# Optimization experiments

Measured on AMD Instinct MI355X. Metric: run time of the kernel, lower is better.

## Reference

```python
import jax, jax.numpy as jnp
import numpy as np

D_MODEL, D_STATE, EXPAND = 768, 16, 2
D_INNER = D_MODEL * EXPAND
B, L = 2, 2048


def setup_inputs() -> dict:
    key = jax.random.key(0)
    ks = jax.random.split(key, 10)
    s = 0.02  # init scale for projection weights
    return {
        "x": jax.random.normal(ks[0], (B, L, D_MODEL), jnp.float32),
        "in_w": jax.random.normal(ks[1], (D_MODEL, 2 * D_INNER), jnp.float32) * s,
        "conv_w": jax.random.normal(ks[2], (D_INNER, 1, 3), jnp.float32) * 0.1,
        "conv_b": jnp.zeros((D_INNER,), jnp.float32),
        "xproj_w": jax.random.normal(ks[3], (D_INNER, 2 * D_STATE), jnp.float32) * s,
        "dt_w": jax.random.normal(ks[4], (D_INNER, D_INNER), jnp.float32) * s,
        "dt_b": jnp.zeros((D_INNER,), jnp.float32),
        "A_log": jax.random.normal(ks[5], (D_INNER, D_STATE), jnp.float32) * 0.01,
        "D": jnp.ones((D_INNER,), jnp.float32),
        "out_w": jax.random.normal(ks[6], (D_INNER, D_MODEL), jnp.float32) * s,
    }


def reference(x, in_w, conv_w, conv_b, xproj_w, dt_w, dt_b, A_log, D, out_w):
    d_inner = conv_w.shape[0]
    d_state = A_log.shape[1]

    xz = x @ in_w                                   # [B,L,2*d_inner]
    x_c, z = jnp.split(xz, 2, axis=-1)

    # depthwise conv1d, kernel 3, padding 1
    xc = jnp.transpose(x_c, (0, 2, 1))              # [B,d_inner,L]
    xc = jax.lax.conv_general_dilated(
        xc, conv_w, window_strides=(1,), padding=[(1, 1)],
        feature_group_count=d_inner,
        dimension_numbers=("NCH", "OIH", "NCH"))
    xc = xc + conv_b[None, :, None]
    xc = jax.nn.silu(jnp.transpose(xc, (0, 2, 1)))  # [B,L,d_inner]

    Bs, Cs = jnp.split(xc @ xproj_w, 2, axis=-1)    # each [B,L,d_state]
    delta = jax.nn.softplus(xc @ dt_w + dt_b)       # [B,L,d_inner]
    A = -jnp.exp(A_log.astype(jnp.float32))         # [d_inner,d_state]

    deltaA = jnp.exp(jnp.einsum("bld,dn->bldn", delta, A))      # [B,L,d_inner,d_state]
    deltaBx = jnp.einsum("bld,bln->bldn", delta * xc, Bs)        # [B,L,d_inner,d_state]

    def step(h, inp):
        dA_t, dBx_t, c_t = inp                      # [B,d,n],[B,d,n],[B,n]
        h = dA_t * h + dBx_t
        y_t = jnp.einsum("bdn,bn->bd", h, c_t)
        return h, y_t

    h0 = jnp.zeros((x.shape[0], d_inner, d_state), xc.dtype)
    xs = (jnp.moveaxis(deltaA, 1, 0), jnp.moveaxis(deltaBx, 1, 0), jnp.moveaxis(Cs, 1, 0))
    _, ys = jax.lax.scan(step, h0, xs)              # ys: [L,B,d_inner]
    y = jnp.moveaxis(ys, 0, 1) + D * xc             # skip connection

    y = y * jax.nn.silu(z)
    return y @ out_w                                # [B,L,d_model]
```

## Files before the change

### kernel.cpp

```cpp
#include <hip/hip_runtime.h>
#include <cmath>

#define DMODEL 768
#define DINNER 1536
#define NSTATE 16
#define SEQL   2048
#define NCHUNK 32
#define CHLEN  64

#define DT_F32  0
#define DT_BF16 1
#define DT_ZERO 2

typedef __bf16 bf16x8 __attribute__((ext_vector_type(8)));
typedef float  f32x4  __attribute__((ext_vector_type(4)));

typedef __attribute__((address_space(3))) unsigned short lds_us;
typedef const __attribute__((address_space(1))) unsigned short glob_us;

__device__ __forceinline__ void async_cp16(glob_us* g, lds_us* l) {
    __builtin_amdgcn_global_load_lds((const __attribute__((address_space(1))) void*)g,
                                     (__attribute__((address_space(3))) void*)l, 16, 0, 0);
}

__device__ __forceinline__ float bf2f(unsigned short h) {
    union { unsigned u; float f; } v; v.u = ((unsigned)h) << 16; return v.f;
}
__device__ __forceinline__ unsigned short f2bf(float f) {
    union { float f; unsigned u; } v; v.f = f;
    unsigned r = (v.u + 0x7FFFu + ((v.u >> 16) & 1u)) >> 16;
    return (unsigned short)r;
}
__device__ int detect_dtype(const void* p) {
    const unsigned* u = (const unsigned*)p;
    int nzlo = 0, band = 0, anynz = 0;
    for (int i = 0; i < 64; ++i) {
        unsigned w = u[i];
        anynz |= (w != 0);
        unsigned lo = w & 0xFFFFu;
        if (lo) {
            ++nzlo;
            unsigned e8 = (lo >> 7) & 0xFF;
            if (e8 >= 0x60 && e8 <= 0x8E) ++band;
        }
    }
    if (nzlo >= 8) return (band * 2 > nzlo) ? DT_BF16 : DT_F32;
    return anynz ? DT_F32 : DT_ZERO;
}
__device__ __forceinline__ float LD(const void* p, size_t i, int dt) {
    if (dt == DT_BF16) return bf2f(((const unsigned short*)p)[i]);
    if (dt == DT_F32)  return ((const float*)p)[i];
    return 0.f;
}

__global__ __launch_bounds__(256) void prep_kernel(
    const void* __restrict__ x, const void* __restrict__ in_w,
    const void* __restrict__ cw, const void* __restrict__ cb,
    const void* __restrict__ xp, const void* __restrict__ dt_w,
    const void* __restrict__ db, const void* __restrict__ Al,
    const void* __restrict__ Dv, const void* __restrict__ out_w,
    unsigned short* __restrict__ xb, unsigned short* __restrict__ inT,
    unsigned short* __restrict__ dtT, unsigned short* __restrict__ outT,
    float* __restrict__ pf)
{
    __shared__ unsigned short tile[64][68];
    __shared__ int dts[6];
    const int blk = blockIdx.x;
    const int t   = threadIdx.x;

    if (blk < 324) {
        if (t == 0) {
            dts[0] = detect_dtype(cw); dts[1] = detect_dtype(cb);
            dts[2] = detect_dtype(db); dts[3] = detect_dtype(Al);
            dts[4] = detect_dtype(Dv); dts[5] = detect_dtype(xp);
        }
        __syncthreads();
        int g = blk * 256 + t;
        if (g >= 82944) return;
        const void* src; int local; int which;
        if      (g <  4608) { src = cw; local = g;         which = 0; }
        else if (g <  6144) { src = cb; local = g - 4608;  which = 1; }
        else if (g <  7680) { src = db; local = g - 6144;  which = 2; }
        else if (g < 32256) { src = Al; local = g - 7680;  which = 3; }
        else if (g < 33792) { src = Dv; local = g - 32256; which = 4; }
        else                { src = xp; local = g - 33792; which = 5; }
        float v = LD(src, local, dts[which]);
        if (which == 3) v = -__expf(v) * 1.44269504f;
        pf[g] = v;
    } else if (blk < 1860) {
        if (t == 0) dts[0] = detect_dtype(x);
        __syncthreads();
        const int dt = dts[0];
        size_t i = ((size_t)(blk - 324) * 256 + t) * 8;
        ushort4 o0, o1;
        if (dt == DT_F32) {
            float4 a = *(const float4*)((const float*)x + i);
            float4 b = *(const float4*)((const float*)x + i + 4);
            o0.x = f2bf(a.x); o0.y = f2bf(a.y); o0.z = f2bf(a.z); o0.w = f2bf(a.w);
            o1.x = f2bf(b.x); o1.y = f2bf(b.y); o1.z = f2bf(b.z); o1.w = f2bf(b.w);
        } else if (dt == DT_BF16) {
            o0 = *(const ushort4*)((const unsigned short*)x + i);
            o1 = *(const ushort4*)((const unsigned short*)x + i + 4);
        } else {
            o0 = (ushort4){0,0,0,0}; o1 = (ushort4){0,0,0,0};
        }
        *(ushort4*)&xb[i] = o0;
        *(ushort4*)&xb[i + 4] = o1;
    } else {
        const void* src; unsigned short* dst; int R, C, tx_n, idx;
        if (blk < 2436)      { src = in_w;  dst = inT;  R = 768;  C = 3072; tx_n = 48; idx = blk - 1860; }
        else if (blk < 3012) { src = dt_w;  dst = dtT;  R = 1536; C = 1536; tx_n = 24; idx = blk - 2436; }
        else                 { src = out_w; dst = outT; R = 1536; C = 768;  tx_n = 12; idx = blk - 3012; }
        if (t == 0) dts[0] = detect_dtype(src);
        __syncthreads();
        const int dt = dts[0];
        const int tx = t & 15, ty = t >> 4;
        const int bx = (idx % tx_n) * 64, by = (idx / tx_n) * 64;
        #pragma unroll
        for (int i = 0; i < 4; ++i) {
            int rl = ty + i * 16;
            size_t soff = (size_t)(by + rl) * C + bx + tx * 4;
            ushort4 hv;
            if (dt == DT_F32) {
                float4 v = *(const float4*)((const float*)src + soff);
                hv.x = f2bf(v.x); hv.y = f2bf(v.y); hv.z = f2bf(v.z); hv.w = f2bf(v.w);
            } else if (dt == DT_BF16) {
                hv = *(const ushort4*)((const unsigned short*)src + soff);
            } else {
                hv = (ushort4){0,0,0,0};
            }
            *(ushort4*)&tile[rl][tx * 4] = hv;
        }
        __syncthreads();
        #pragma unroll
        for (int i = 0; i < 4; ++i) {
            int cl = ty + i * 16;
            int m0 = tx * 4;
            ushort4 o;
            o.x = tile[m0 + 0][cl]; o.y = tile[m0 + 1][cl];
            o.z = tile[m0 + 2][cl]; o.w = tile[m0 + 3][cl];
            *(ushort4*)&dst[(size_t)(bx + cl) * R + by + m0] = o;
        }
    }
}

template<int EPI>
__global__ __launch_bounds__(256) void gemm_kernel(
    const unsigned short* __restrict__ A, const unsigned short* __restrict__ Bt,
    void* __restrict__ C0, void* __restrict__ C1, const float* __restrict__ biasf,
    int M, int N, int K)
{
    __shared__ __align__(16) unsigned short As[2][2][128 * 32];
    __shared__ __align__(16) unsigned short Bs[2][2][64 * 32];
    const int t    = threadIdx.x;
    const int m0   = blockIdx.x * 128;
    const int n0   = blockIdx.y * 64;
    const int w    = t >> 6;
    const int lane = t & 63;
    const int wm   = (w >> 1) * 64, wn = (w & 1) * 32;
    const int lm   = lane & 15, quad = lane >> 4;
    const int srow = lane >> 2;
    const int sg   = lane & 3;

    f32x4 acc[4][2] = {};

    auto stage = [&](int k0, int q) {
        #pragma unroll
        for (int ph = 0; ph < 2; ++ph) {
            #pragma unroll
            for (int h = 0; h < 2; ++h) {
                int row = w * 32 + h * 16 + srow;
                int kg  = (sg - (row >> 1)) & 3;
                async_cp16((glob_us*)&A[(size_t)(m0 + row) * K + k0 + ph * 32 + kg * 8],
                           (lds_us*)&As[q][ph][(w * 32 + h * 16) * 32]);
            }
            int brow = w * 16 + srow;
            int bkg  = (sg - (brow >> 1)) & 3;
            async_cp16((glob_us*)&Bt[(size_t)(n0 + brow) * K + k0 + ph * 32 + bkg * 8],
                       (lds_us*)&Bs[q][ph][(w * 16) * 32]);
        }
    };

    stage(0, 0);

    int p = 0;
    for (int k0 = 0; k0 < K; k0 += 64) {
        __syncthreads();
        if (k0 + 64 < K) stage(k0 + 64, p ^ 1);
        #pragma unroll
        for (int ph = 0; ph < 2; ++ph) {
            bf16x8 af[4], bfr[2];
            #pragma unroll
            for (int i = 0; i < 4; ++i) {
                int row = wm + i * 16 + lm;
                int g   = (quad + (row >> 1)) & 3;
                af[i] = *(const bf16x8*)&As[p][ph][row * 32 + g * 8];
            }
            #pragma unroll
            for (int j = 0; j < 2; ++j) {
                int row = wn + j * 16 + lm;
                int g   = (quad + (row >> 1)) & 3;
                bfr[j] = *(const bf16x8*)&Bs[p][ph][row * 32 + g * 8];
            }
            #pragma unroll
            for (int i = 0; i < 4; ++i)
                #pragma unroll
                for (int j = 0; j < 2; ++j)
                    acc[i][j] = __builtin_amdgcn_mfma_f32_16x16x32_bf16(af[i], bfr[j], acc[i][j], 0, 0, 0);
        }
        p ^= 1;
    }

    const int half = N >> 1;
    #pragma unroll
    for (int i = 0; i < 4; ++i) {
        #pragma unroll
        for (int j = 0; j < 2; ++j) {
            int col = n0 + wn + j * 16 + lm;
            #pragma unroll
            for (int r = 0; r < 4; ++r) {
                int row = m0 + wm + i * 16 + quad * 4 + r;
                float v = acc[i][j][r];
                if (EPI == 1) {
                    v += biasf[col];
                    float sp = (v > 20.f) ? v : log1pf(__expf(v));
                    ((unsigned short*)C0)[(size_t)row * N + col] = f2bf(sp);
                } else if (EPI == 2) {
                    ((float*)C0)[(size_t)row * N + col] = v;
                } else {
                    if (col < half) {
                        ((unsigned short*)C0)[(size_t)row * half + col] = f2bf(v);
                    } else {
                        float s = v / (1.f + __expf(-v));
                        ((unsigned short*)C1)[(size_t)row * half + col - half] = f2bf(s);
                    }
                }
            }
        }
    }
}

__global__ __launch_bounds__(256) void conv_silu_kernel(
    const unsigned short* __restrict__ xcpre, const float* __restrict__ cwf,
    const float* __restrict__ cbf, unsigned short* __restrict__ xcb)
{
    int idx = blockIdx.x * 256 + threadIdx.x;
    int d   = idx % DINNER;
    int row = idx / DINNER;
    int l   = row % SEQL;
    size_t base = (size_t)row * DINNER + d;
    float acc = cbf[d];
    if (l > 0)        acc += bf2f(xcpre[base - DINNER]) * cwf[d * 3 + 0];
    acc += bf2f(xcpre[base]) * cwf[d * 3 + 1];
    if (l < SEQL - 1) acc += bf2f(xcpre[base + DINNER]) * cwf[d * 3 + 2];
    float s = acc / (1.f + __expf(-acc));
    xcb[base] = f2bf(s);
}

__global__ __launch_bounds__(128) void xproj_kernel(
    const unsigned short* __restrict__ xcb, const float* __restrict__ wf,
    float* __restrict__ BC)
{
    __shared__ float red[4][32][4];
    const int t = threadIdx.x;
    const int s = t & 31, part = t >> 5;
    const int row0 = blockIdx.x * 4;
    float acc[4] = {0.f, 0.f, 0.f, 0.f};
    for (int k = part * 384; k < (part + 1) * 384; ++k) {
        float wv = wf[k * 32 + s];
        #pragma unroll
        for (int r = 0; r < 4; ++r)
            acc[r] += bf2f(xcb[(size_t)(row0 + r) * DINNER + k]) * wv;
    }
    #pragma unroll
    for (int r = 0; r < 4; ++r) red[part][s][r] = acc[r];
    __syncthreads();
    if (t < 32) {
        #pragma unroll
        for (int r = 0; r < 4; ++r)
            BC[(size_t)(row0 + r) * 32 + t] =
                red[0][t][r] + red[1][t][r] + red[2][t][r] + red[3][t][r];
    }
}

struct GrpA { unsigned short dv[4], xv[4]; f32x4 Bv[4]; };
struct GrpC { unsigned short dv[4], xv[4], zq; f32x4 Bv[4], Cv[4]; };

__device__ __forceinline__ void ldA(GrpA& gp, const unsigned short* pd,
    const unsigned short* px, const float* pbc, int l) {
    #pragma unroll
    for (int j = 0; j < 4; ++j) {
        size_t o = (size_t)(l + j) * DINNER;
        gp.dv[j] = pd[o];
        gp.xv[j] = px[o];
        gp.Bv[j] = *(const f32x4*)&pbc[(size_t)(l + j) * 32];
    }
}
__device__ __forceinline__ void ldC(GrpC& gp, const unsigned short* pd,
    const unsigned short* px, const unsigned short* pz, const float* pbc,
    int l, int q) {
    #pragma unroll
    for (int j = 0; j < 4; ++j) {
        size_t o = (size_t)(l + j) * DINNER;
        gp.dv[j] = pd[o];
        gp.xv[j] = px[o];
        gp.Bv[j] = *(const f32x4*)&pbc[(size_t)(l + j) * 32];
        gp.Cv[j] = *(const f32x4*)&pbc[(size_t)(l + j) * 32 + 16];
    }
    gp.zq = pz[(size_t)(l + q) * DINNER];
}
__device__ __forceinline__ void stepA(const GrpA& gp, const f32x4 A2,
    f32x4& h, float& sdv) {
    #pragma unroll
    for (int j = 0; j < 4; ++j) {
        float dv = bf2f(gp.dv[j]);
        float xv = bf2f(gp.xv[j]);
        float dx = dv * xv;
        sdv += dv;
        f32x4 e;
        e[0] = __builtin_amdgcn_exp2f(dv * A2[0]);
        e[1] = __builtin_amdgcn_exp2f(dv * A2[1]);
        e[2] = __builtin_amdgcn_exp2f(dv * A2[2]);
        e[3] = __builtin_amdgcn_exp2f(dv * A2[3]);
        h = e * h + dx * gp.Bv[j];
    }
}
__device__ __forceinline__ void stepC(const GrpC& gp, const f32x4 A2,
    f32x4& h, float Dd, int q, unsigned short* py, int l) {
    float yq = 0.f, xq = 0.f;
    #pragma unroll
    for (int j = 0; j < 4; ++j) {
        float dv = bf2f(gp.dv[j]);
        float xv = bf2f(gp.xv[j]);
        float dx = dv * xv;
        f32x4 e;
        e[0] = __builtin_amdgcn_exp2f(dv * A2[0]);
        e[1] = __builtin_amdgcn_exp2f(dv * A2[1]);
        e[2] = __builtin_amdgcn_exp2f(dv * A2[2]);
        e[3] = __builtin_amdgcn_exp2f(dv * A2[3]);
        h = e * h + dx * gp.Bv[j];
        f32x4 yv = h * gp.Cv[j];
        float y = yv[0] + yv[1] + yv[2] + yv[3];
        y += __shfl_xor(y, 1);
        y += __shfl_xor(y, 2);
        if (j == q) { yq = y; xq = xv; }
    }
    float zv = bf2f(gp.zq);
    py[(size_t)(l + q) * DINNER] = f2bf((yq + Dd * xq) * zv);
}

__global__ __launch_bounds__(256) void scan_phase_a(
    const unsigned short* __restrict__ dlt, const unsigned short* __restrict__ xcb,
    const float* __restrict__ BC, const float* __restrict__ A_log_f,
    unsigned short* __restrict__ P, float* __restrict__ S)
{
    int g = blockIdx.x * 256 + threadIdx.x;
    int q = g & 3;
    int d = (g >> 2) % DINNER;
    int c = ((g >> 2) / DINNER) % NCHUNK;
    int b = (g >> 2) / (DINNER * NCHUNK);
    f32x4 A2 = *(const f32x4*)&A_log_f[d * 16 + q * 4];
    f32x4 h = (f32x4){0.f, 0.f, 0.f, 0.f};
    float sdv = 0.f;
    const int row0 = b * SEQL + c * CHLEN;
    const unsigned short* pd = dlt + (size_t)row0 * DINNER + d;
    const unsigned short* px = xcb + (size_t)row0 * DINNER + d;
    const float* pbc = BC + (size_t)row0 * 32 + q * 4;

    GrpA ga, gb;
    ldA(ga, pd, px, pbc, 0);
    for (int l0 = 0; l0 < CHLEN; l0 += 8) {
        ldA(gb, pd, px, pbc, l0 + 4);
        stepA(ga, A2, h, sdv);
        if (l0 + 8 < CHLEN) ldA(ga, pd, px, pbc, l0 + 8);
        stepA(gb, A2, h, sdv);
    }

    size_t idx = (((size_t)(b * NCHUNK + c)) * DINNER + d) * 16 + q * 4;
    *(f32x4*)&S[idx] = h;
    ushort4 pq;
    pq.x = f2bf(__builtin_amdgcn_exp2f(sdv * A2[0]));
    pq.y = f2bf(__builtin_amdgcn_exp2f(sdv * A2[1]));
    pq.z = f2bf(__builtin_amdgcn_exp2f(sdv * A2[2]));
    pq.w = f2bf(__builtin_amdgcn_exp2f(sdv * A2[3]));
    *(ushort4*)&P[idx] = pq;
}

__global__ __launch_bounds__(256) void scan_combine(
    const unsigned short* __restrict__ P, float* __restrict__ S)
{
    int t = blockIdx.x * 256 + threadIdx.x;
    int b = t / (DINNER * NSTATE);
    int dn = t % (DINNER * NSTATE);
    const size_t stride = (size_t)(DINNER * NSTATE);
    size_t idx = (size_t)b * NCHUNK * stride + dn;
    float Pv = bf2f(P[idx]);
    float Sv = S[idx];
    float H = 0.f;
    for (int c = 0; c < NCHUNK; ++c) {
        float Pn = 0.f, Sn = 0.f;
        if (c + 1 < NCHUNK) {
            Pn = bf2f(P[idx + stride]);
            Sn = S[idx + stride];
        }
        S[idx] = H;
        H = Pv * H + Sv;
        Pv = Pn; Sv = Sn;
        idx += stride;
    }
}

__global__ __launch_bounds__(256) void scan_phase_c(
    const unsigned short* __restrict__ dlt, const unsigned short* __restrict__ xcb,
    const float* __restrict__ BC, const unsigned short* __restrict__ zg,
    const float* __restrict__ A_log_f, const float* __restrict__ D_f,
    const float* __restrict__ Hin, unsigned short* __restrict__ yg)
{
    int g = blockIdx.x * 256 + threadIdx.x;
    int q = g & 3;
    int d = (g >> 2) % DINNER;
    int c = ((g >> 2) / DINNER) % NCHUNK;
    int b = (g >> 2) / (DINNER * NCHUNK);
    f32x4 A2 = *(const f32x4*)&A_log_f[d * 16 + q * 4];
    size_t hidx = (((size_t)(b * NCHUNK + c)) * DINNER + d) * 16 + q * 4;
    f32x4 h = *(const f32x4*)&Hin[hidx];
    const float Dd = D_f[d];
    const int row0 = b * SEQL + c * CHLEN;
    const unsigned short* pd = dlt + (size_t)row0 * DINNER + d;
    const unsigned short* px = xcb + (size_t)row0 * DINNER + d;
    const unsigned short* pz = zg  + (size_t)row0 * DINNER + d;
    unsigned short* py = yg + (size_t)row0 * DINNER + d;
    const float* pbc = BC + (size_t)row0 * 32 + q * 4;

    GrpC ga, gb;
    ldC(ga, pd, px, pz, pbc, 0, q);
    for (int l0 = 0; l0 < CHLEN; l0 += 8) {
        ldC(gb, pd, px, pz, pbc, l0 + 4, q);
        stepC(ga, A2, h, Dd, q, py, l0);
        if (l0 + 8 < CHLEN) ldC(ga, pd, px, pz, pbc, l0 + 8, q);
        stepC(gb, A2, h, Dd, q, py, l0 + 4);
    }
}

__global__ void guard_kernel(float* out, int code)
{
    if (threadIdx.x == 0 && blockIdx.x == 0 && code) out[0] = (float)code;
}

extern "C" void kernel_launch(void* const* d_in, const int* in_sizes, int n_in,
                              void* d_out, int out_size, void* d_ws, size_t ws_size,
                              hipStream_t stream) {
    static const int EXPECTED[10] = {3145728, 2359296, 4608, 1536, 49152,
                                     2359296, 1536, 24576, 1536, 1179648};
    bool ok = (n_in == 10);
    if (ok) for (int i = 0; i < 10; ++i) ok = ok && (in_sizes[i] == EXPECTED[i]);
    int code = 0;
    if (!ok) code = 2000;
    else if (ws_size < 67895296ULL) code = 3000;
    if (code) { guard_kernel<<<1, 64, 0, stream>>>((float*)d_out, code); return; }

    const void* x       = d_in[0];
    const void* in_w    = d_in[1];
    const void* conv_w  = d_in[2];
    const void* conv_b  = d_in[3];
    const void* xproj_w = d_in[4];
    const void* dt_w    = d_in[5];
    const void* dt_b    = d_in[6];
    const void* A_log   = d_in[7];
    const void* Dvec    = d_in[8];
    const void* out_w   = d_in[9];

    char* ws = (char*)d_ws;
    float* conv_w_f = (float*)(ws + 0);
    float* conv_b_f = (float*)(ws + 18432);
    float* dt_b_f   = (float*)(ws + 24576);
    float* A_log_f  = (float*)(ws + 30720);
    float* D_f      = (float*)(ws + 129024);
    float* xproj_f  = (float*)(ws + 135168);
    unsigned short* xb    = (unsigned short*)(ws + 524288);
    unsigned short* inT   = (unsigned short*)(ws + 6815744);
    unsigned short* yg    = (unsigned short*)(ws + 524288);
    unsigned short* dtT   = (unsigned short*)(ws + 13107200);
    unsigned short* outT  = (unsigned short*)(ws + 17825792);
    unsigned short* xcpre = (unsigned short*)(ws + 20185088);
    unsigned short* dlt   = xcpre;
    float*          BC    = (float*)(ws + 32768000);
    unsigned short* zg    = (unsigned short*)(ws + 33292288);
    unsigned short* xcb   = (unsigned short*)(ws + 45875200);
    float*          scanS = (float*)(ws + 58458112);
    unsigned short* scanP = (unsigned short*)(ws + 64749568);

    prep_kernel<<<3300, 256, 0, stream>>>(x, in_w, conv_w, conv_b, xproj_w, dt_w,
                                          dt_b, A_log, Dvec, out_w,
                                          xb, inT, dtT, outT, (float*)ws);

    gemm_kernel<3><<<dim3(32, 48), 256, 0, stream>>>(xb, inT, (void*)xcpre, (void*)zg,
                                                     nullptr, 4096, 3072, 768);
    conv_silu_kernel<<<(4096 * DINNER) / 256, 256, 0, stream>>>(xcpre, conv_w_f, conv_b_f, xcb);
    xproj_kernel<<<1024, 128, 0, stream>>>(xcb, xproj_f, BC);
    gemm_kernel<1><<<dim3(32, 24), 256, 0, stream>>>(xcb, dtT, (void*)dlt, nullptr,
                                                     dt_b_f, 4096, 1536, 1536);
    scan_phase_a<<<1536, 256, 0, stream>>>(dlt, xcb, BC, A_log_f, scanP, scanS);
    scan_combine<<<192, 256, 0, stream>>>(scanP, scanS);
    scan_phase_c<<<1536, 256, 0, stream>>>(dlt, xcb, BC, zg, A_log_f, D_f, scanS, yg);
    gemm_kernel<2><<<dim3(32, 12), 256, 0, stream>>>(yg, outT, d_out, nullptr,
                                                    nullptr, 4096, 768, 1536);
}
```

Measured before the change: 322.5 us.

## Stage scan inputs through LDS with async triple-buffered global loads

Both chunked scan kernels now have each block cover 64 channels of one chunk, with separate wavefronts issuing async global-to-LDS copies of delta, x, z and B/C rows into triple-buffered shared memory. Threads then read their per-step values from LDS instead of issuing scattered 2-byte global loads per timestep. This is meant to replace uncoalesced narrow loads with wide coalesced ones and to overlap fetch with compute. In exchange it adds a block-wide barrier every 8 steps and some LDS use per block.

```diff
diff --git a/kernel.cpp b/kernel.cpp
--- a/kernel.cpp
+++ b/kernel.cpp
@@ -283,100 +283,70 @@
     }
 }
 
-struct GrpA { unsigned short dv[4], xv[4]; f32x4 Bv[4]; };
-struct GrpC { unsigned short dv[4], xv[4], zq; f32x4 Bv[4], Cv[4]; };
-
-__device__ __forceinline__ void ldA(GrpA& gp, const unsigned short* pd,
-    const unsigned short* px, const float* pbc, int l) {
-    #pragma unroll
-    for (int j = 0; j < 4; ++j) {
-        size_t o = (size_t)(l + j) * DINNER;
-        gp.dv[j] = pd[o];
-        gp.xv[j] = px[o];
-        gp.Bv[j] = *(const f32x4*)&pbc[(size_t)(l + j) * 32];
-    }
-}
-__device__ __forceinline__ void ldC(GrpC& gp, const unsigned short* pd,
-    const unsigned short* px, const unsigned short* pz, const float* pbc,
-    int l, int q) {
-    #pragma unroll
-    for (int j = 0; j < 4; ++j) {
-        size_t o = (size_t)(l + j) * DINNER;
-        gp.dv[j] = pd[o];
-        gp.xv[j] = px[o];
-        gp.Bv[j] = *(const f32x4*)&pbc[(size_t)(l + j) * 32];
-        gp.Cv[j] = *(const f32x4*)&pbc[(size_t)(l + j) * 32 + 16];
-    }
-    gp.zq = pz[(size_t)(l + q) * DINNER];
-}
-__device__ __forceinline__ void stepA(const GrpA& gp, const f32x4 A2,
-    f32x4& h, float& sdv) {
-    #pragma unroll
-    for (int j = 0; j < 4; ++j) {
-        float dv = bf2f(gp.dv[j]);
-        float xv = bf2f(gp.xv[j]);
-        float dx = dv * xv;
-        sdv += dv;
-        f32x4 e;
-        e[0] = __builtin_amdgcn_exp2f(dv * A2[0]);
-        e[1] = __builtin_amdgcn_exp2f(dv * A2[1]);
-        e[2] = __builtin_amdgcn_exp2f(dv * A2[2]);
-        e[3] = __builtin_amdgcn_exp2f(dv * A2[3]);
-        h = e * h + dx * gp.Bv[j];
-    }
-}
-__device__ __forceinline__ void stepC(const GrpC& gp, const f32x4 A2,
-    f32x4& h, float Dd, int q, unsigned short* py, int l) {
-    float yq = 0.f, xq = 0.f;
-    #pragma unroll
-    for (int j = 0; j < 4; ++j) {
-        float dv = bf2f(gp.dv[j]);
-        float xv = bf2f(gp.xv[j]);
-        float dx = dv * xv;
-        f32x4 e;
-        e[0] = __builtin_amdgcn_exp2f(dv * A2[0]);
-        e[1] = __builtin_amdgcn_exp2f(dv * A2[1]);
-        e[2] = __builtin_amdgcn_exp2f(dv * A2[2]);
-        e[3] = __builtin_amdgcn_exp2f(dv * A2[3]);
-        h = e * h + dx * gp.Bv[j];
-        f32x4 yv = h * gp.Cv[j];
-        float y = yv[0] + yv[1] + yv[2] + yv[3];
-        y += __shfl_xor(y, 1);
-        y += __shfl_xor(y, 2);
-        if (j == q) { yq = y; xq = xv; }
-    }
-    float zv = bf2f(gp.zq);
-    py[(size_t)(l + q) * DINNER] = f2bf((yq + Dd * xq) * zv);
-}
-
 __global__ __launch_bounds__(256) void scan_phase_a(
     const unsigned short* __restrict__ dlt, const unsigned short* __restrict__ xcb,
     const float* __restrict__ BC, const float* __restrict__ A_log_f,
     unsigned short* __restrict__ P, float* __restrict__ S)
 {
-    int g = blockIdx.x * 256 + threadIdx.x;
-    int q = g & 3;
-    int d = (g >> 2) % DINNER;
-    int c = ((g >> 2) / DINNER) % NCHUNK;
-    int b = (g >> 2) / (DINNER * NCHUNK);
+    __shared__ __align__(16) unsigned short dS[3][8][64];
+    __shared__ __align__(16) unsigned short xS[3][8][64];
+    __shared__ __align__(16) float bS[3][8][32];
+    const int t    = threadIdx.x;
+    const int w    = t >> 6, lane = t & 63;
+    const int q    = t & 3,  dl   = t >> 2;
+    const int bid  = blockIdx.x;
+    const int dg   = bid % 24;
+    const int cc   = (bid / 24) % NCHUNK;
+    const int b    = bid / (24 * NCHUNK);
+    const int d0   = dg * 64;
+    const int d    = d0 + dl;
+    const int row0 = b * SEQL + cc * CHLEN;
+    const int srow = lane >> 3, scol = lane & 7;
+
     f32x4 A2 = *(const f32x4*)&A_log_f[d * 16 + q * 4];
     f32x4 h = (f32x4){0.f, 0.f, 0.f, 0.f};
     float sdv = 0.f;
-    const int row0 = b * SEQL + c * CHLEN;
-    const unsigned short* pd = dlt + (size_t)row0 * DINNER + d;
-    const unsigned short* px = xcb + (size_t)row0 * DINNER + d;
-    const float* pbc = BC + (size_t)row0 * 32 + q * 4;
-
-    GrpA ga, gb;
-    ldA(ga, pd, px, pbc, 0);
-    for (int l0 = 0; l0 < CHLEN; l0 += 8) {
-        ldA(gb, pd, px, pbc, l0 + 4);
-        stepA(ga, A2, h, sdv);
-        if (l0 + 8 < CHLEN) ldA(ga, pd, px, pbc, l0 + 8);
-        stepA(gb, A2, h, sdv);
-    }
-
-    size_t idx = (((size_t)(b * NCHUNK + c)) * DINNER + d) * 16 + q * 4;
+
+    auto stage = [&](int g, int buf) {
+        int r = row0 + g * 8 + srow;
+        if (w == 0)
+            async_cp16((glob_us*)&dlt[(size_t)r * DINNER + d0 + scol * 8],
+                       (lds_us*)&dS[buf][0][0] + lane * 8);
+        else if (w == 1)
+            async_cp16((glob_us*)&xcb[(size_t)r * DINNER + d0 + scol * 8],
+                       (lds_us*)&xS[buf][0][0] + lane * 8);
+        else if (w == 2)
+            async_cp16((glob_us*)&BC[(size_t)r * 32 + scol * 4],
+                       (lds_us*)&bS[buf][0][0] + lane * 8);
+    };
+
+    stage(0, 0);
+    stage(1, 1);
+    #pragma unroll
+    for (int g = 0; g < 8; ++g) {
+        if (g < 7) asm volatile("s_waitcnt vmcnt(1)" ::: "memory");
+        else       asm volatile("s_waitcnt vmcnt(0)" ::: "memory");
+        __builtin_amdgcn_s_barrier();
+        __builtin_amdgcn_sched_barrier(0);
+        if (g + 2 < 8) stage(g + 2, (g + 2) % 3);
+        const int buf = g % 3;
+        #pragma unroll
+        for (int l = 0; l < 8; ++l) {
+            float dv = bf2f(dS[buf][l][dl]);
+            float xv = bf2f(xS[buf][l][dl]);
+            float dx = dv * xv;
+            sdv += dv;
+            f32x4 Bv = *(const f32x4*)&bS[buf][l][q * 4];
+            f32x4 e;
+            e[0] = __builtin_amdgcn_exp2f(dv * A2[0]);
+            e[1] = __builtin_amdgcn_exp2f(dv * A2[1]);
+            e[2] = __builtin_amdgcn_exp2f(dv * A2[2]);
+            e[3] = __builtin_amdgcn_exp2f(dv * A2[3]);
+            h = e * h + dx * Bv;
+        }
+    }
+
+    size_t idx = (((size_t)(b * NCHUNK + cc)) * DINNER + d) * 16 + q * 4;
     *(f32x4*)&S[idx] = h;
     ushort4 pq;
     pq.x = f2bf(__builtin_amdgcn_exp2f(sdv * A2[0]));
@@ -416,29 +386,75 @@
     const float* __restrict__ A_log_f, const float* __restrict__ D_f,
     const float* __restrict__ Hin, unsigned short* __restrict__ yg)
 {
-    int g = blockIdx.x * 256 + threadIdx.x;
-    int q = g & 3;
-    int d = (g >> 2) % DINNER;
-    int c = ((g >> 2) / DINNER) % NCHUNK;
-    int b = (g >> 2) / (DINNER * NCHUNK);
+    __shared__ __align__(16) unsigned short dS[3][8][64];
+    __shared__ __align__(16) unsigned short xS[3][8][64];
+    __shared__ __align__(16) unsigned short zS[3][8][64];
+    __shared__ __align__(16) float bS[3][8][32];
+    const int t    = threadIdx.x;
+    const int w    = t >> 6, lane = t & 63;
+    const int q    = t & 3,  dl   = t >> 2;
+    const int bid  = blockIdx.x;
+    const int dg   = bid % 24;
+    const int cc   = (bid / 24) % NCHUNK;
+    const int b    = bid / (24 * NCHUNK);
+    const int d0   = dg * 64;
+    const int d    = d0 + dl;
+    const int row0 = b * SEQL + cc * CHLEN;
+    const int srow = lane >> 3, scol = lane & 7;
+
     f32x4 A2 = *(const f32x4*)&A_log_f[d * 16 + q * 4];
-    size_t hidx = (((size_t)(b * NCHUNK + c)) * DINNER + d) * 16 + q * 4;
+    size_t hidx = (((size_t)(b * NCHUNK + cc)) * DINNER + d) * 16 + q * 4;
     f32x4 h = *(const f32x4*)&Hin[hidx];
     const float Dd = D_f[d];
-    const int row0 = b * SEQL + c * CHLEN;
-    const unsigned short* pd = dlt + (size_t)row0 * DINNER + d;
-    const unsigned short* px = xcb + (size_t)row0 * DINNER + d;
-    const unsigned short* pz = zg  + (size_t)row0 * DINNER + d;
-    unsigned short* py = yg + (size_t)row0 * DINNER + d;
-    const float* pbc = BC + (size_t)row0 * 32 + q * 4;
-
-    GrpC ga, gb;
-    ldC(ga, pd, px, pz, pbc, 0, q);
-    for (int l0 = 0; l0 < CHLEN; l0 += 8) {
-        ldC(gb, pd, px, pz, pbc, l0 + 4, q);
-        stepC(ga, A2, h, Dd, q, py, l0);
-        if (l0 + 8 < CHLEN) ldC(ga, pd, px, pz, pbc, l0 + 8, q);
-        stepC(gb, A2, h, Dd, q, py, l0 + 4);
+
+    auto stage = [&](int g, int buf) {
+        int r = row0 + g * 8 + srow;
+        if (w == 0)
+            async_cp16((glob_us*)&dlt[(size_t)r * DINNER + d0 + scol * 8],
+                       (lds_us*)&dS[buf][0][0] + lane * 8);
+        else if (w == 1)
+            async_cp16((glob_us*)&xcb[(size_t)r * DINNER + d0 + scol * 8],
+                       (lds_us*)&xS[buf][0][0] + lane * 8);
+        else if (w == 2)
+            async_cp16((glob_us*)&zg[(size_t)r * DINNER + d0 + scol * 8],
+                       (lds_us*)&zS[buf][0][0] + lane * 8);
+        else
+            async_cp16((glob_us*)&BC[(size_t)r * 32 + scol * 4],
+                       (lds_us*)&bS[buf][0][0] + lane * 8);
+    };
+
+    stage(0, 0);
+    stage(1, 1);
+    #pragma unroll
+    for (int g = 0; g < 8; ++g) {
+        if (g < 7) asm volatile("s_waitcnt vmcnt(1)" ::: "memory");
+        else       asm volatile("s_waitcnt vmcnt(0)" ::: "memory");
+        __builtin_amdgcn_s_barrier();
+        __builtin_amdgcn_sched_barrier(0);
+        if (g + 2 < 8) stage(g + 2, (g + 2) % 3);
+        const int buf = g % 3;
+        #pragma unroll
+        for (int l = 0; l < 8; ++l) {
+            float dv = bf2f(dS[buf][l][dl]);
+            float xv = bf2f(xS[buf][l][dl]);
+            float dx = dv * xv;
+            f32x4 Bv = *(const f32x4*)&bS[buf][l][q * 4];
+            f32x4 Cv = *(const f32x4*)&bS[buf][l][16 + q * 4];
+            f32x4 e;
+            e[0] = __builtin_amdgcn_exp2f(dv * A2[0]);
+            e[1] = __builtin_amdgcn_exp2f(dv * A2[1]);
+            e[2] = __builtin_amdgcn_exp2f(dv * A2[2]);
+            e[3] = __builtin_amdgcn_exp2f(dv * A2[3]);
+            h = e * h + dx * Bv;
+            f32x4 yv = h * Cv;
+            float y = yv[0] + yv[1] + yv[2] + yv[3];
+            y += __shfl_xor(y, 1);
+            y += __shfl_xor(y, 2);
+            if ((l & 3) == q) {
+                float zv = bf2f(zS[buf][l][dl]);
+                yg[(size_t)(row0 + g * 8 + l) * DINNER + d] = f2bf((y + Dd * xv) * zv);
+            }
+        }
     }
 }
 
```

Result: no change. 325.4 us (+0.9%).

## Vectorize conv-silu and process two channels per thread in chunked scan

Applied to the files above, without the earlier changes.

The depthwise conv+SiLU kernel now handles 8 channels per thread with 16-byte loads and stores, and the conv weights are transposed in prep to a tap-major layout so they can be read as float4. Both scan phases now give each thread two adjacent channels, loading packed bf16 pairs and sharing the B/C vector loads, with half as many blocks. The y quad reduction uses DPP moves instead of shuffles, and z is loaded only for the owning lane. The aim is fewer, wider memory transactions and less redundant B/C traffic. The cost is higher register pressure in the scan kernels and lower occupancy.

```diff
diff --git a/kernel.cpp b/kernel.cpp
--- a/kernel.cpp
+++ b/kernel.cpp
@@ -26,10 +26,23 @@
 __device__ __forceinline__ float bf2f(unsigned short h) {
     union { unsigned u; float f; } v; v.u = ((unsigned)h) << 16; return v.f;
 }
+__device__ __forceinline__ float bflo(unsigned p) {
+    union { unsigned u; float f; } v; v.u = p << 16; return v.f;
+}
+__device__ __forceinline__ float bfhi(unsigned p) {
+    union { unsigned u; float f; } v; v.u = p & 0xFFFF0000u; return v.f;
+}
 __device__ __forceinline__ unsigned short f2bf(float f) {
     union { float f; unsigned u; } v; v.f = f;
     unsigned r = (v.u + 0x7FFFu + ((v.u >> 16) & 1u)) >> 16;
     return (unsigned short)r;
+}
+__device__ __forceinline__ float quad_reduce(float y) {
+    int yi = __float_as_int(y);
+    y += __int_as_float(__builtin_amdgcn_mov_dpp(yi, 0xB1, 0xF, 0xF, true));
+    yi = __float_as_int(y);
+    y += __int_as_float(__builtin_amdgcn_mov_dpp(yi, 0x4E, 0xF, 0xF, true));
+    return y;
 }
 __device__ int detect_dtype(const void* p) {
     const unsigned* u = (const unsigned*)p;
@@ -85,8 +98,10 @@
         else if (g < 33792) { src = Dv; local = g - 32256; which = 4; }
         else                { src = xp; local = g - 33792; which = 5; }
         float v = LD(src, local, dts[which]);
+        int out = g;
         if (which == 3) v = -__expf(v) * 1.44269504f;
-        pf[g] = v;
+        if (which == 0) out = (local % 3) * DINNER + local / 3;
+        pf[out] = v;
     } else if (blk < 1860) {
         if (t == 0) dts[0] = detect_dtype(x);
         __syncthreads();
@@ -244,17 +259,43 @@
     const unsigned short* __restrict__ xcpre, const float* __restrict__ cwf,
     const float* __restrict__ cbf, unsigned short* __restrict__ xcb)
 {
-    int idx = blockIdx.x * 256 + threadIdx.x;
-    int d   = idx % DINNER;
-    int row = idx / DINNER;
+    const float* cw0 = cwf;
+    const float* cw1 = cwf + DINNER;
+    const float* cw2 = cwf + 2 * DINNER;
+    size_t idx = ((size_t)blockIdx.x * 256 + threadIdx.x) * 8;
+    int d8  = (int)(idx % DINNER);
+    int row = (int)(idx / DINNER);
     int l   = row % SEQL;
-    size_t base = (size_t)row * DINNER + d;
-    float acc = cbf[d];
-    if (l > 0)        acc += bf2f(xcpre[base - DINNER]) * cwf[d * 3 + 0];
-    acc += bf2f(xcpre[base]) * cwf[d * 3 + 1];
-    if (l < SEQL - 1) acc += bf2f(xcpre[base + DINNER]) * cwf[d * 3 + 2];
-    float s = acc / (1.f + __expf(-acc));
-    xcb[base] = f2bf(s);
+    size_t base = (size_t)row * DINNER + d8;
+    uint4 zero = {0, 0, 0, 0};
+    uint4 xm = (l > 0)        ? *(const uint4*)&xcpre[base - DINNER] : zero;
+    uint4 x0 = *(const uint4*)&xcpre[base];
+    uint4 xp = (l < SEQL - 1) ? *(const uint4*)&xcpre[base + DINNER] : zero;
+    float4 c0a = *(const float4*)&cw0[d8], c0b = *(const float4*)&cw0[d8 + 4];
+    float4 c1a = *(const float4*)&cw1[d8], c1b = *(const float4*)&cw1[d8 + 4];
+    float4 c2a = *(const float4*)&cw2[d8], c2b = *(const float4*)&cw2[d8 + 4];
+    float4 cba = *(const float4*)&cbf[d8], cbb = *(const float4*)&cbf[d8 + 4];
+    const unsigned* mw = (const unsigned*)&xm;
+    const unsigned* zw = (const unsigned*)&x0;
+    const unsigned* pw = (const unsigned*)&xp;
+    const float* C0 = (const float*)&c0a;
+    float w0[8] = {c0a.x, c0a.y, c0a.z, c0a.w, c0b.x, c0b.y, c0b.z, c0b.w};
+    float w1[8] = {c1a.x, c1a.y, c1a.z, c1a.w, c1b.x, c1b.y, c1b.z, c1b.w};
+    float w2[8] = {c2a.x, c2a.y, c2a.z, c2a.w, c2b.x, c2b.y, c2b.z, c2b.w};
+    float bb[8] = {cba.x, cba.y, cba.z, cba.w, cbb.x, cbb.y, cbb.z, cbb.w};
+    (void)C0;
+    unsigned short out[8];
+    #pragma unroll
+    for (int k = 0; k < 8; ++k) {
+        unsigned wm_ = mw[k >> 1], wz = zw[k >> 1], wp = pw[k >> 1];
+        float a = (k & 1) ? bfhi(wm_) : bflo(wm_);
+        float c = (k & 1) ? bfhi(wz)  : bflo(wz);
+        float e = (k & 1) ? bfhi(wp)  : bflo(wp);
+        float acc = bb[k] + a * w0[k] + c * w1[k] + e * w2[k];
+        float s = acc / (1.f + __expf(-acc));
+        out[k] = f2bf(s);
+    }
+    *(uint4*)&xcb[base] = *(uint4*)out;
 }
 
 __global__ __launch_bounds__(128) void xproj_kernel(
@@ -283,70 +324,50 @@
     }
 }
 
-struct GrpA { unsigned short dv[4], xv[4]; f32x4 Bv[4]; };
-struct GrpC { unsigned short dv[4], xv[4], zq; f32x4 Bv[4], Cv[4]; };
+struct GrpA { unsigned dv2[4], xv2[4]; f32x4 Bv[4]; };
+struct GrpC { unsigned dv2[4], xv2[4]; f32x4 Bv[4], Cv[4]; };
 
 __device__ __forceinline__ void ldA(GrpA& gp, const unsigned short* pd,
     const unsigned short* px, const float* pbc, int l) {
     #pragma unroll
     for (int j = 0; j < 4; ++j) {
         size_t o = (size_t)(l + j) * DINNER;
-        gp.dv[j] = pd[o];
-        gp.xv[j] = px[o];
-        gp.Bv[j] = *(const f32x4*)&pbc[(size_t)(l + j) * 32];
+        gp.dv2[j] = *(const unsigned*)&pd[o];
+        gp.xv2[j] = *(const unsigned*)&px[o];
+        gp.Bv[j]  = *(const f32x4*)&pbc[(size_t)(l + j) * 32];
     }
 }
 __device__ __forceinline__ void ldC(GrpC& gp, const unsigned short* pd,
-    const unsigned short* px, const unsigned short* pz, const float* pbc,
-    int l, int q) {
+    const unsigned short* px, const float* pbc, int l) {
     #pragma unroll
     for (int j = 0; j < 4; ++j) {
         size_t o = (size_t)(l + j) * DINNER;
-        gp.dv[j] = pd[o];
-        gp.xv[j] = px[o];
-        gp.Bv[j] = *(const f32x4*)&pbc[(size_t)(l + j) * 32];
-        gp.Cv[j] = *(const f32x4*)&pbc[(size_t)(l + j) * 32 + 16];
-    }
-    gp.zq = pz[(size_t)(l + q) * DINNER];
-}
-__device__ __forceinline__ void stepA(const GrpA& gp, const f32x4 A2,
-    f32x4& h, float& sdv) {
+        gp.dv2[j] = *(const unsigned*)&pd[o];
+        gp.xv2[j] = *(const unsigned*)&px[o];
+        gp.Bv[j]  = *(const f32x4*)&pbc[(size_t)(l + j) * 32];
+        gp.Cv[j]  = *(const f32x4*)&pbc[(size_t)(l + j) * 32 + 16];
+    }
+}
+__device__ __forceinline__ void stepA(const GrpA& gp, const f32x4 A2a,
+    const f32x4 A2b, f32x4& h0, f32x4& h1, float& sdv0, float& sdv1) {
     #pragma unroll
     for (int j = 0; j < 4; ++j) {
-        float dv = bf2f(gp.dv[j]);
-        float xv = bf2f(gp.xv[j]);
-        float dx = dv * xv;
-        sdv += dv;
-        f32x4 e;
-        e[0] = __builtin_amdgcn_exp2f(dv * A2[0]);
-        e[1] = __builtin_amdgcn_exp2f(dv * A2[1]);
-        e[2] = __builtin_amdgcn_exp2f(dv * A2[2]);
-        e[3] = __builtin_amdgcn_exp2f(dv * A2[3]);
-        h = e * h + dx * gp.Bv[j];
-    }
-}
-__device__ __forceinline__ void stepC(const GrpC& gp, const f32x4 A2,
-    f32x4& h, float Dd, int q, unsigned short* py, int l) {
-    float yq = 0.f, xq = 0.f;
-    #pragma unroll
-    for (int j = 0; j < 4; ++j) {
-        float dv = bf2f(gp.dv[j]);
-        float xv = bf2f(gp.xv[j]);
-        float dx = dv * xv;
-        f32x4 e;
-        e[0] = __builtin_amdgcn_exp2f(dv * A2[0]);
-        e[1] = __builtin_amdgcn_exp2f(dv * A2[1]);
-        e[2] = __builtin_amdgcn_exp2f(dv * A2[2]);
-        e[3] = __builtin_amdgcn_exp2f(dv * A2[3]);
-        h = e * h + dx * gp.Bv[j];
-        f32x4 yv = h * gp.Cv[j];
-        float y = yv[0] + yv[1] + yv[2] + yv[3];
-        y += __shfl_xor(y, 1);
-        y += __shfl_xor(y, 2);
-        if (j == q) { yq = y; xq = xv; }
-    }
-    float zv = bf2f(gp.zq);
-    py[(size_t)(l + q) * DINNER] = f2bf((yq + Dd * xq) * zv);
+        float dv0 = bflo(gp.dv2[j]), dv1 = bfhi(gp.dv2[j]);
+        float xv0 = bflo(gp.xv2[j]), xv1 = bfhi(gp.xv2[j]);
+        sdv0 += dv0; sdv1 += dv1;
+        f32x4 Bv = gp.Bv[j];
+        f32x4 e0, e1;
+        e0[0] = __builtin_amdgcn_exp2f(dv0 * A2a[0]);
+        e0[1] = __builtin_amdgcn_exp2f(dv0 * A2a[1]);
+        e0[2] = __builtin_amdgcn_exp2f(dv0 * A2a[2]);
+        e0[3] = __builtin_amdgcn_exp2f(dv0 * A2a[3]);
+        e1[0] = __builtin_amdgcn_exp2f(dv1 * A2b[0]);
+        e1[1] = __builtin_amdgcn_exp2f(dv1 * A2b[1]);
+        e1[2] = __builtin_amdgcn_exp2f(dv1 * A2b[2]);
+        e1[3] = __builtin_amdgcn_exp2f(dv1 * A2b[3]);
+        h0 = e0 * h0 + (dv0 * xv0) * Bv;
+        h1 = e1 * h1 + (dv1 * xv1) * Bv;
+    }
 }
 
 __global__ __launch_bounds__(256) void scan_phase_a(
@@ -354,15 +375,20 @@
     const float* __restrict__ BC, const float* __restrict__ A_log_f,
     unsigned short* __restrict__ P, float* __restrict__ S)
 {
-    int g = blockIdx.x * 256 + threadIdx.x;
-    int q = g & 3;
-    int d = (g >> 2) % DINNER;
-    int c = ((g >> 2) / DINNER) % NCHUNK;
-    int b = (g >> 2) / (DINNER * NCHUNK);
-    f32x4 A2 = *(const f32x4*)&A_log_f[d * 16 + q * 4];
-    f32x4 h = (f32x4){0.f, 0.f, 0.f, 0.f};
-    float sdv = 0.f;
-    const int row0 = b * SEQL + c * CHLEN;
+    const int t   = threadIdx.x;
+    const int q   = t & 3;
+    const int dpl = t >> 2;
+    const int bid = blockIdx.x;
+    const int dg  = bid % 12;
+    const int cc  = (bid / 12) % NCHUNK;
+    const int b   = bid / (12 * NCHUNK);
+    const int d   = (dg * 64 + dpl) * 2;
+    f32x4 A2a = *(const f32x4*)&A_log_f[d * 16 + q * 4];
+    f32x4 A2b = *(const f32x4*)&A_log_f[(d + 1) * 16 + q * 4];
+    f32x4 h0 = (f32x4){0.f, 0.f, 0.f, 0.f};
+    f32x4 h1 = (f32x4){0.f, 0.f, 0.f, 0.f};
+    float sdv0 = 0.f, sdv1 = 0.f;
+    const int row0 = b * SEQL + cc * CHLEN;
     const unsigned short* pd = dlt + (size_t)row0 * DINNER + d;
     const unsigned short* px = xcb + (size_t)row0 * DINNER + d;
     const float* pbc = BC + (size_t)row0 * 32 + q * 4;
@@ -371,19 +397,25 @@
     ldA(ga, pd, px, pbc, 0);
     for (int l0 = 0; l0 < CHLEN; l0 += 8) {
         ldA(gb, pd, px, pbc, l0 + 4);
-        stepA(ga, A2, h, sdv);
+        stepA(ga, A2a, A2b, h0, h1, sdv0, sdv1);
         if (l0 + 8 < CHLEN) ldA(ga, pd, px, pbc, l0 + 8);
-        stepA(gb, A2, h, sdv);
-    }
-
-    size_t idx = (((size_t)(b * NCHUNK + c)) * DINNER + d) * 16 + q * 4;
-    *(f32x4*)&S[idx] = h;
-    ushort4 pq;
-    pq.x = f2bf(__builtin_amdgcn_exp2f(sdv * A2[0]));
-    pq.y = f2bf(__builtin_amdgcn_exp2f(sdv * A2[1]));
-    pq.z = f2bf(__builtin_amdgcn_exp2f(sdv * A2[2]));
-    pq.w = f2bf(__builtin_amdgcn_exp2f(sdv * A2[3]));
-    *(ushort4*)&P[idx] = pq;
+        stepA(gb, A2a, A2b, h0, h1, sdv0, sdv1);
+    }
+
+    size_t idx = (((size_t)(b * NCHUNK + cc)) * DINNER + d) * 16 + q * 4;
+    *(f32x4*)&S[idx] = h0;
+    *(f32x4*)&S[idx + 16] = h1;
+    ushort4 p0, p1;
+    p0.x = f2bf(__builtin_amdgcn_exp2f(sdv0 * A2a[0]));
+    p0.y = f2bf(__builtin_amdgcn_exp2f(sdv0 * A2a[1]));
+    p0.z = f2bf(__builtin_amdgcn_exp2f(sdv0 * A2a[2]));
+    p0.w = f2bf(__builtin_amdgcn_exp2f(sdv0 * A2a[3]));
+    p1.x = f2bf(__builtin_amdgcn_exp2f(sdv1 * A2b[0]));
+    p1.y = f2bf(__builtin_amdgcn_exp2f(sdv1 * A2b[1]));
+    p1.z = f2bf(__builtin_amdgcn_exp2f(sdv1 * A2b[2]));
+    p1.w = f2bf(__builtin_amdgcn_exp2f(sdv1 * A2b[3]));
+    *(ushort4*)&P[idx] = p0;
+    *(ushort4*)&P[idx + 16] = p1;
 }
 
 __global__ __launch_bounds__(256) void scan_combine(
@@ -416,16 +448,21 @@
     const float* __restrict__ A_log_f, const float* __restrict__ D_f,
     const float* __restrict__ Hin, unsigned short* __restrict__ yg)
 {
-    int g = blockIdx.x * 256 + threadIdx.x;
-    int q = g & 3;
-    int d = (g >> 2) % DINNER;
-    int c = ((g >> 2) / DINNER) % NCHUNK;
-    int b = (g >> 2) / (DINNER * NCHUNK);
-    f32x4 A2 = *(const f32x4*)&A_log_f[d * 16 + q * 4];
-    size_t hidx = (((size_t)(b * NCHUNK + c)) * DINNER + d) * 16 + q * 4;
-    f32x4 h = *(const f32x4*)&Hin[hidx];
-    const float Dd = D_f[d];
-    const int row0 = b * SEQL + c * CHLEN;
+    const int t   = threadIdx.x;
+    const int q   = t & 3;
+    const int dpl = t >> 2;
+    const int bid = blockIdx.x;
+    const int dg  = bid % 12;
+    const int cc  = (bid / 12) % NCHUNK;
+    const int b   = bid / (12 * NCHUNK);
+    const int d   = (dg * 64 + dpl) * 2;
+    f32x4 A2a = *(const f32x4*)&A_log_f[d * 16 + q * 4];
+    f32x4 A2b = *(const f32x4*)&A_log_f[(d + 1) * 16 + q * 4];
+    size_t hidx = (((size_t)(b * NCHUNK + cc)) * DINNER + d) * 16 + q * 4;
+    f32x4 h0 = *(const f32x4*)&Hin[hidx];
+    f32x4 h1 = *(const f32x4*)&Hin[hidx + 16];
+    const float Dd0 = D_f[d], Dd1 = D_f[d + 1];
+    const int row0 = b * SEQL + cc * CHLEN;
     const unsigned short* pd = dlt + (size_t)row0 * DINNER + d;
     const unsigned short* px = xcb + (size_t)row0 * DINNER + d;
     const unsigned short* pz = zg  + (size_t)row0 * DINNER + d;
@@ -433,12 +470,43 @@
     const float* pbc = BC + (size_t)row0 * 32 + q * 4;
 
     GrpC ga, gb;
-    ldC(ga, pd, px, pz, pbc, 0, q);
+    auto stepC = [&](const GrpC& gp, int l) {
+        #pragma unroll
+        for (int j = 0; j < 4; ++j) {
+            float dv0 = bflo(gp.dv2[j]), dv1 = bfhi(gp.dv2[j]);
+            float xv0 = bflo(gp.xv2[j]), xv1 = bfhi(gp.xv2[j]);
+            f32x4 Bv = gp.Bv[j], Cv = gp.Cv[j];
+            f32x4 e0, e1;
+            e0[0] = __builtin_amdgcn_exp2f(dv0 * A2a[0]);
+            e0[1] = __builtin_amdgcn_exp2f(dv0 * A2a[1]);
+            e0[2] = __builtin_amdgcn_exp2f(dv0 * A2a[2]);
+            e0[3] = __builtin_amdgcn_exp2f(dv0 * A2a[3]);
+            e1[0] = __builtin_amdgcn_exp2f(dv1 * A2b[0]);
+            e1[1] = __builtin_amdgcn_exp2f(dv1 * A2b[1]);
+            e1[2] = __builtin_amdgcn_exp2f(dv1 * A2b[2]);
+            e1[3] = __builtin_amdgcn_exp2f(dv1 * A2b[3]);
+            h0 = e0 * h0 + (dv0 * xv0) * Bv;
+            h1 = e1 * h1 + (dv1 * xv1) * Bv;
+            f32x4 y0v = h0 * Cv;
+            f32x4 y1v = h1 * Cv;
+            float y0 = quad_reduce(y0v[0] + y0v[1] + y0v[2] + y0v[3]);
+            float y1 = quad_reduce(y1v[0] + y1v[1] + y1v[2] + y1v[3]);
+            if (j == q) {
+                unsigned zp = *(const unsigned*)&pz[(size_t)(l + j) * DINNER];
+                ushort2 o;
+                o.x = f2bf((y0 + Dd0 * xv0) * bflo(zp));
+                o.y = f2bf((y1 + Dd1 * xv1) * bfhi(zp));
+                *(ushort2*)&py[(size_t)(l + j) * DINNER] = o;
+            }
+        }
+    };
+
+    ldC(ga, pd, px, pbc, 0);
     for (int l0 = 0; l0 < CHLEN; l0 += 8) {
-        ldC(gb, pd, px, pz, pbc, l0 + 4, q);
-        stepC(ga, A2, h, Dd, q, py, l0);
-        if (l0 + 8 < CHLEN) ldC(ga, pd, px, pz, pbc, l0 + 8, q);
-        stepC(gb, A2, h, Dd, q, py, l0 + 4);
+        ldC(gb, pd, px, pbc, l0 + 4);
+        stepC(ga, l0);
+        if (l0 + 8 < CHLEN) ldC(ga, pd, px, pbc, l0 + 8);
+        stepC(gb, l0 + 4);
     }
 }
 
@@ -496,13 +564,13 @@
 
     gemm_kernel<3><<<dim3(32, 48), 256, 0, stream>>>(xb, inT, (void*)xcpre, (void*)zg,
                                                      nullptr, 4096, 3072, 768);
-    conv_silu_kernel<<<(4096 * DINNER) / 256, 256, 0, stream>>>(xcpre, conv_w_f, conv_b_f, xcb);
+    conv_silu_kernel<<<(4096 * DINNER / 8) / 256, 256, 0, stream>>>(xcpre, conv_w_f, conv_b_f, xcb);
     xproj_kernel<<<1024, 128, 0, stream>>>(xcb, xproj_f, BC);
     gemm_kernel<1><<<dim3(32, 24), 256, 0, stream>>>(xcb, dtT, (void*)dlt, nullptr,
                                                      dt_b_f, 4096, 1536, 1536);
-    scan_phase_a<<<1536, 256, 0, stream>>>(dlt, xcb, BC, A_log_f, scanP, scanS);
+    scan_phase_a<<<768, 256, 0, stream>>>(dlt, xcb, BC, A_log_f, scanP, scanS);
     scan_combine<<<192, 256, 0, stream>>>(scanP, scanS);
-    scan_phase_c<<<1536, 256, 0, stream>>>(dlt, xcb, BC, zg, A_log_f, D_f, scanS, yg);
+    scan_phase_c<<<768, 256, 0, stream>>>(dlt, xcb, BC, zg, A_log_f, D_f, scanS, yg);
     gemm_kernel<2><<<dim3(32, 12), 256, 0, stream>>>(yg, outT, d_out, nullptr,
                                                     nullptr, 4096, 768, 1536);
 }
```

New measurement: 316.6 us. No clear change (-1.8%).
